# Kernel optimization log

Measured on AMD Instinct MI355X. Metric: run time of the kernel, lower is better.

Reference implementation:

```python
import jax, jax.numpy as jnp
import numpy as np

H = 1024   # hidden size
E = 8      # num experts
B, S = 4, 2048


def setup_inputs() -> dict:
    key = jax.random.key(0)
    k1, k2, k3, k4 = jax.random.split(key, 4)
    x = jax.random.normal(k1, (B, S, H), dtype=jnp.float32)
    wg = jax.random.normal(k2, (H, E), dtype=jnp.float32) * 0.02      # gate weight
    W = jax.random.normal(k3, (E, H, H), dtype=jnp.float32) * 0.02    # expert Linear weights (out, in) per expert
    b = jax.random.normal(k4, (E, H), dtype=jnp.float32) * 0.02       # expert Linear biases
    return {"x": x, "wg": wg, "W": W, "b": b}


def reference(x, wg, W, b):
    Bb, Ss, Hh = x.shape
    Ee = wg.shape[1]
    T = Bb * Ss
    C = T // Ee  # capacity (capacity_factor = 1.0, top-1)

    xt = x.reshape(T, Hh)
    logits = xt @ wg                                   # [T, E]
    probs = jax.nn.softmax(logits, axis=-1)            # [T, E]
    idx = jnp.argmax(probs, axis=-1)                   # [T] top-1 expert
    mask = jax.nn.one_hot(idx, Ee, dtype=xt.dtype)     # [T, E]

    # position of each token within its expert's queue (0-based)
    locations = jnp.cumsum(mask, axis=0) - mask        # [T, E]
    # drop tokens over capacity
    mask = mask * (locations < C).astype(xt.dtype)
    gate = jnp.sum(probs * mask, axis=-1)              # [T] gate prob (0 if dropped)
    loc_s = jnp.sum(locations * mask, axis=-1).astype(jnp.int32)  # [T]
    loc_oh = jax.nn.one_hot(loc_s, C, dtype=xt.dtype)  # [T, C]

    dispatch = mask[:, :, None] * loc_oh[:, None, :]   # [T, E, C]
    combine = gate[:, None, None] * dispatch           # [T, E, C]

    # dispatch tokens -> per-expert buffers [E, C, H]
    exp_in = jnp.einsum('tec,th->ech', dispatch, xt)
    # per-expert Linear: y = x @ W_e^T + b_e
    exp_out = jnp.einsum('ech,efh->ecf', exp_in, W) + b[:, None, :]
    # combine back to tokens, scaled by gate prob
    out = jnp.einsum('tec,ecf->tf', combine, exp_out)  # [T, H]
    return out.reshape(Bb, Ss, Hh)
```

## Files before the change

### kernel.cpp

```cpp
#include <hip/hip_runtime.h>

#define H 1024
#define E 8
#define T 8192
#define CAP 1024

typedef __bf16 bf16x8 __attribute__((ext_vector_type(8)));
typedef float  f32x4  __attribute__((ext_vector_type(4)));
typedef unsigned short u16;

__device__ __forceinline__ u16 f2bf(float f) {
    union { float f; unsigned u; } v; v.f = f;
    unsigned r = v.u + 0x7FFFu + ((v.u >> 16) & 1u);
    return (u16)(r >> 16);
}

typedef __attribute__((address_space(1))) const void* gas_t;
typedef __attribute__((address_space(3))) void* las_t;
__device__ __forceinline__ void gld16(const void* g, void* l) {
    __builtin_amdgcn_global_load_lds((gas_t)g, (las_t)l, 16, 0, 0);
}

__global__ __launch_bounds__(256) void wgt_kernel(
    const float* __restrict__ wg, float* __restrict__ wgT) {
    const int h = blockIdx.x * 256 + threadIdx.x;
    float4 lo = *(const float4*)(wg + h * E);
    float4 hi = *(const float4*)(wg + h * E + 4);
    wgT[0 * H + h] = lo.x; wgT[1 * H + h] = lo.y;
    wgT[2 * H + h] = lo.z; wgT[3 * H + h] = lo.w;
    wgT[4 * H + h] = hi.x; wgT[5 * H + h] = hi.y;
    wgT[6 * H + h] = hi.z; wgT[7 * H + h] = hi.w;
}

#define GATE_BLOCKS 512
#define CVT_BLOCKS  1536

__global__ __launch_bounds__(256) void gatecvt_kernel(
    const float* __restrict__ x, const float* __restrict__ wgT,
    const float* __restrict__ W,
    int* __restrict__ eid, float* __restrict__ gate,
    u16* __restrict__ xbf, u16* __restrict__ Wbf) {
    const int tid = threadIdx.x;

    if (blockIdx.x >= GATE_BLOCKS) {
        int i = (blockIdx.x - GATE_BLOCKS) * 256 + tid;
        const int n4 = E * H * H / 4;
        const int stride = CVT_BLOCKS * 256;
        for (; i < n4; i += stride) {
            float4 v = ((const float4*)W)[i];
            ushort4 o;
            o.x = f2bf(v.x); o.y = f2bf(v.y); o.z = f2bf(v.z); o.w = f2bf(v.w);
            ((ushort4*)Wbf)[i] = o;
        }
        return;
    }

    const int wv = tid >> 6, lane = tid & 63;
    const int tbase = blockIdx.x * 16 + wv * 4;
    const int h00 = lane * 4;

    float a[4][8];
    #pragma unroll
    for (int j = 0; j < 4; ++j)
        #pragma unroll
        for (int e = 0; e < 8; ++e) a[j][e] = 0.f;

    #pragma unroll
    for (int q = 0; q < 4; ++q) {
        const int h0 = q * 256 + h00;
        float4 xv[4];
        #pragma unroll
        for (int j = 0; j < 4; ++j)
            xv[j] = *(const float4*)(x + (size_t)(tbase + j) * H + h0);
        #pragma unroll
        for (int j = 0; j < 4; ++j) {
            ushort4 o;
            o.x = f2bf(xv[j].x); o.y = f2bf(xv[j].y);
            o.z = f2bf(xv[j].z); o.w = f2bf(xv[j].w);
            *(ushort4*)(xbf + (size_t)(tbase + j) * H + h0) = o;
        }
        #pragma unroll
        for (int e = 0; e < 8; ++e) {
            const float4 w4 = *(const float4*)(wgT + e * H + h0);
            #pragma unroll
            for (int j = 0; j < 4; ++j)
                a[j][e] += xv[j].x * w4.x + xv[j].y * w4.y
                         + xv[j].z * w4.z + xv[j].w * w4.w;
        }
    }

    const bool b0 = lane & 1, b1 = lane & 2, b2 = lane & 4;
    const int elane = ((lane & 1) << 2) | (lane & 2) | ((lane >> 2) & 1);

    #pragma unroll
    for (int j = 0; j < 4; ++j) {
        float* A = a[j];
        #pragma unroll
        for (int k = 0; k < 4; ++k) {
            float t = b0 ? A[k] : A[k + 4];
            t = __shfl_xor(t, 1);
            A[k] = (b0 ? A[k + 4] : A[k]) + t;
        }
        #pragma unroll
        for (int k = 0; k < 2; ++k) {
            float t = b1 ? A[k] : A[k + 2];
            t = __shfl_xor(t, 2);
            A[k] = (b1 ? A[k + 2] : A[k]) + t;
        }
        {
            float t = b2 ? A[0] : A[1];
            t = __shfl_xor(t, 4);
            A[0] = (b2 ? A[1] : A[0]) + t;
        }
        float v = A[0];
        v += __shfl_xor(v, 8); v += __shfl_xor(v, 16); v += __shfl_xor(v, 32);
        float m = v; int mi = elane;
        #pragma unroll
        for (int off = 1; off <= 4; off <<= 1) {
            float om = __shfl_xor(m, off);
            int   oi = __shfl_xor(mi, off);
            if (om > m || (om == m && oi < mi)) { m = om; mi = oi; }
        }
        float s = expf(v - m);
        s += __shfl_xor(s, 1); s += __shfl_xor(s, 2); s += __shfl_xor(s, 4);
        if (lane == 0) {
            eid[tbase + j]  = mi;
            gate[tbase + j] = 1.0f / s;
        }
    }
}

#define TPT 32
__global__ __launch_bounds__(256) void scan_kernel(
    const int* __restrict__ eid, float* __restrict__ gate,
    int* __restrict__ perm) {
    __shared__ int cnt[256][E];
    __shared__ int base[256][E];
    __shared__ int part[E][8];
    const int tid = threadIdx.x;

    for (int i = tid; i < E * CAP; i += 256) perm[i] = -1;

    const int t0 = tid * TPT;
    int c[E];
    #pragma unroll
    for (int e = 0; e < E; ++e) c[e] = 0;
    for (int i = 0; i < TPT; ++i) {
        const int ei = eid[t0 + i];
        #pragma unroll
        for (int e = 0; e < E; ++e) c[e] += (ei == e);
    }
    #pragma unroll
    for (int e = 0; e < E; ++e) cnt[tid][e] = c[e];
    __syncthreads();
    if (tid < 64) {
        const int e = tid >> 3, j = tid & 7;
        int s = 0;
        for (int i = j * 32; i < j * 32 + 32; ++i) s += cnt[i][e];
        part[e][j] = s;
    }
    __syncthreads();
    if (tid < E) {
        int run = 0;
        #pragma unroll
        for (int j = 0; j < 8; ++j) { int v = part[tid][j]; part[tid][j] = run; run += v; }
    }
    __syncthreads();
    if (tid < 64) {
        const int e = tid >> 3, j = tid & 7;
        int run = part[e][j];
        for (int i = j * 32; i < j * 32 + 32; ++i) { base[i][e] = run; run += cnt[i][e]; }
    }
    __syncthreads();
    #pragma unroll
    for (int e = 0; e < E; ++e) c[e] = base[tid][e];
    for (int i = 0; i < TPT; ++i) {
        const int t = t0 + i;
        const int ei = eid[t];
        int pos = 0;
        #pragma unroll
        for (int e = 0; e < E; ++e) if (ei == e) pos = c[e]++;
        if (pos < CAP) perm[ei * CAP + pos] = t;
        else gate[t] = 0.f;
    }
}

__global__ __launch_bounds__(512, 4) void moe_gemm_bf(
    const u16* __restrict__ xbf, const u16* __restrict__ Wbf,
    const float* __restrict__ bias, const int* __restrict__ perm,
    const float* __restrict__ gate, float* __restrict__ out) {
    __shared__ __align__(16) u16 As[2][128 * 64];
    __shared__ __align__(16) u16 Bs[2][128 * 64];
    __shared__ int   perm_s[128];
    __shared__ float gate_s[128];

    const int tid = threadIdx.x;
    const int idx = blockIdx.x;

    if (idx >= 512) {
        const int t = (idx - 512) * 128 + (tid >> 2);
        if (gate[t] == 0.f) {
            const int part = tid & 3;
            float4 z = make_float4(0.f, 0.f, 0.f, 0.f);
            float4* o = (float4*)(out + (size_t)t * H + part * 256);
            #pragma unroll
            for (int i = 0; i < 64; ++i) o[i] = z;
        }
        return;
    }

    const int fb = idx >> 6;
    const int mb = (idx >> 3) & 7;
    const int e  = idx & 7;

    if (tid < 128) {
        const int t = perm[e * CAP + mb * 128 + tid];
        perm_s[tid] = t;
        gate_s[tid] = (t >= 0) ? gate[t] : 0.f;
    }
    __syncthreads();

    const int lane = tid & 63;
    const int wv = tid >> 6;
    const int wm = wv >> 2;
    const int wn = wv & 3;
    const int l16 = lane & 15, quad = lane >> 4;

    const int rl  = lane >> 3;
    const int cch = lane & 7;
    const int gch = cch ^ rl;
    const u16* ga[2]; const u16* gb[2];
    #pragma unroll
    for (int q = 0; q < 2; ++q) {
        const int r = wv * 16 + q * 8 + rl;
        const int tA = perm_s[r];
        const int tok = tA >= 0 ? tA : 0;
        ga[q] = xbf + (size_t)tok * H + gch * 8;
        gb[q] = Wbf + (size_t)e * H * H + (size_t)(fb * 128 + r) * H + gch * 8;
    }

    f32x4 acc[4][2] = {};

    for (int kt = 0; kt < H / 128; ++kt) {
        __syncthreads();
        #pragma unroll
        for (int hb = 0; hb < 2; ++hb)
            #pragma unroll
            for (int q = 0; q < 2; ++q) {
                u16* la = &As[hb][(wv * 16 + q * 8) * 64 + lane * 8];
                u16* lb = &Bs[hb][(wv * 16 + q * 8) * 64 + lane * 8];
                gld16(ga[q] + hb * 64, la);
                gld16(gb[q] + hb * 64, lb);
            }
        #pragma unroll
        for (int q = 0; q < 2; ++q) { ga[q] += 128; gb[q] += 128; }
        __syncthreads();
        #pragma unroll
        for (int hb = 0; hb < 2; ++hb)
            #pragma unroll
            for (int s = 0; s < 2; ++s) {
                bf16x8 af[4], bfr[2];
                const int cc = (s * 4 + quad) ^ (l16 & 7);
                #pragma unroll
                for (int i = 0; i < 4; ++i)
                    af[i] = *(const bf16x8*)&As[hb][(wm * 64 + i * 16 + l16) * 64 + cc * 8];
                #pragma unroll
                for (int i = 0; i < 2; ++i)
                    bfr[i] = *(const bf16x8*)&Bs[hb][(wn * 32 + i * 16 + l16) * 64 + cc * 8];
                #pragma unroll
                for (int mi = 0; mi < 4; ++mi)
                    #pragma unroll
                    for (int ni = 0; ni < 2; ++ni)
                        acc[mi][ni] = __builtin_amdgcn_mfma_f32_16x16x32_bf16(
                            af[mi], bfr[ni], acc[mi][ni], 0, 0, 0);
            }
    }

    float bv[2];
    #pragma unroll
    for (int ni = 0; ni < 2; ++ni)
        bv[ni] = bias[e * H + fb * 128 + wn * 32 + ni * 16 + l16];

    #pragma unroll
    for (int mi = 0; mi < 4; ++mi) {
        #pragma unroll
        for (int r = 0; r < 4; ++r) {
            const int rowl = wm * 64 + mi * 16 + quad * 4 + r;
            const int t = perm_s[rowl];
            if (t < 0) continue;
            const float g = gate_s[rowl];
            float* orow = out + (size_t)t * H + fb * 128 + wn * 32;
            #pragma unroll
            for (int ni = 0; ni < 2; ++ni)
                orow[ni * 16 + l16] = g * (acc[mi][ni][r] + bv[ni]);
        }
    }
}

extern "C" void kernel_launch(void* const* d_in, const int* in_sizes, int n_in,
                              void* d_out, int out_size, void* d_ws, size_t ws_size,
                              hipStream_t stream) {
    const float* x    = (const float*)d_in[0];
    const float* wg   = (const float*)d_in[1];
    const float* W    = (const float*)d_in[2];
    const float* bias = (const float*)d_in[3];
    float* out = (float*)d_out;

    int*   eid  = (int*)d_ws;
    float* gate = (float*)((char*)d_ws + (size_t)T * 4);
    int*   perm = (int*)((char*)d_ws + (size_t)T * 8);
    float* wgT  = (float*)((char*)d_ws + (size_t)T * 12);
    u16*   xbf  = (u16*)((char*)d_ws + (size_t)T * 12 + (size_t)E * H * 4);
    u16*   Wbf  = xbf + (size_t)T * H;

    wgt_kernel<<<H / 256, 256, 0, stream>>>(wg, wgT);
    gatecvt_kernel<<<GATE_BLOCKS + CVT_BLOCKS, 256, 0, stream>>>(
        x, wgT, W, eid, gate, xbf, Wbf);
    scan_kernel<<<1, 256, 0, stream>>>(eid, gate, perm);
    moe_gemm_bf<<<512 + 64, 512, 0, stream>>>(xbf, Wbf, bias, perm, gate, out);
}
```

Measured before the change: 152.5 us.

## Convert expert weights to bf16 inside GEMM and drop separate conversion pass

Removes the standalone fp32-to-bf16 conversion of the 32 MB expert weight tensor. The GEMM now loads fp32 weights into registers one k-tile ahead, packs them with v_cvt_pk_bf16_f32 and stores them to LDS, which avoids writing and re-reading a 16 MB bf16 copy. The gate weight transpose is folded into the gate kernel through shared memory, the scan is widened to 1024 threads, and the zero-fill blocks are moved to the front of the grid. Each weight tile is now read as fp32 once per token block (8 m-blocks per expert), which doubles B-side global traffic and adds register pressure and conversion work inside the GEMM loop.

```diff
diff --git a/kernel.cpp b/kernel.cpp
--- a/kernel.cpp
+++ b/kernel.cpp
@@ -15,45 +15,43 @@
     return (u16)(r >> 16);
 }
 
+__device__ __forceinline__ unsigned cvt2bf(float lo, float hi) {
+    unsigned r;
+    asm("v_cvt_pk_bf16_f32 %0, %1, %2" : "=v"(r) : "v"(lo), "v"(hi));
+    return r;
+}
+
 typedef __attribute__((address_space(1))) const void* gas_t;
 typedef __attribute__((address_space(3))) void* las_t;
 __device__ __forceinline__ void gld16(const void* g, void* l) {
     __builtin_amdgcn_global_load_lds((gas_t)g, (las_t)l, 16, 0, 0);
 }
 
-__global__ __launch_bounds__(256) void wgt_kernel(
-    const float* __restrict__ wg, float* __restrict__ wgT) {
-    const int h = blockIdx.x * 256 + threadIdx.x;
-    float4 lo = *(const float4*)(wg + h * E);
-    float4 hi = *(const float4*)(wg + h * E + 4);
-    wgT[0 * H + h] = lo.x; wgT[1 * H + h] = lo.y;
-    wgT[2 * H + h] = lo.z; wgT[3 * H + h] = lo.w;
-    wgT[4 * H + h] = hi.x; wgT[5 * H + h] = hi.y;
-    wgT[6 * H + h] = hi.z; wgT[7 * H + h] = hi.w;
-}
-
-#define GATE_BLOCKS 512
-#define CVT_BLOCKS  1536
-
-__global__ __launch_bounds__(256) void gatecvt_kernel(
-    const float* __restrict__ x, const float* __restrict__ wgT,
-    const float* __restrict__ W,
-    int* __restrict__ eid, float* __restrict__ gate,
-    u16* __restrict__ xbf, u16* __restrict__ Wbf) {
+__global__ __launch_bounds__(256) void gate_kernel(
+    const float* __restrict__ x, const float* __restrict__ wg,
+    int* __restrict__ eid, float* __restrict__ gate, u16* __restrict__ xbf) {
+    __shared__ float wgs[E][H];
     const int tid = threadIdx.x;
 
-    if (blockIdx.x >= GATE_BLOCKS) {
-        int i = (blockIdx.x - GATE_BLOCKS) * 256 + tid;
-        const int n4 = E * H * H / 4;
-        const int stride = CVT_BLOCKS * 256;
-        for (; i < n4; i += stride) {
-            float4 v = ((const float4*)W)[i];
-            ushort4 o;
-            o.x = f2bf(v.x); o.y = f2bf(v.y); o.z = f2bf(v.z); o.w = f2bf(v.w);
-            ((ushort4*)Wbf)[i] = o;
-        }
-        return;
-    }
+    {
+        const int h0 = tid * 4;
+        float4 lo[4], hi[4];
+        #pragma unroll
+        for (int r = 0; r < 4; ++r) {
+            const float4* p = (const float4*)(wg + (size_t)(h0 + r) * E);
+            lo[r] = p[0]; hi[r] = p[1];
+        }
+        #pragma unroll
+        for (int e = 0; e < 4; ++e) {
+            float4 v0 = make_float4(((const float*)&lo[0])[e], ((const float*)&lo[1])[e],
+                                    ((const float*)&lo[2])[e], ((const float*)&lo[3])[e]);
+            *(float4*)&wgs[e][h0] = v0;
+            float4 v1 = make_float4(((const float*)&hi[0])[e], ((const float*)&hi[1])[e],
+                                    ((const float*)&hi[2])[e], ((const float*)&hi[3])[e]);
+            *(float4*)&wgs[e + 4][h0] = v1;
+        }
+    }
+    __syncthreads();
 
     const int wv = tid >> 6, lane = tid & 63;
     const int tbase = blockIdx.x * 16 + wv * 4;
@@ -81,7 +79,7 @@
         }
         #pragma unroll
         for (int e = 0; e < 8; ++e) {
-            const float4 w4 = *(const float4*)(wgT + e * H + h0);
+            const float4 w4 = *(const float4*)&wgs[e][h0];
             #pragma unroll
             for (int j = 0; j < 4; ++j)
                 a[j][e] += xv[j].x * w4.x + xv[j].y * w4.y
@@ -130,63 +128,68 @@
     }
 }
 
-#define TPT 32
-__global__ __launch_bounds__(256) void scan_kernel(
+#define SCAN_T 1024
+#define STPT 8
+__global__ __launch_bounds__(1024) void scan_kernel(
     const int* __restrict__ eid, float* __restrict__ gate,
     int* __restrict__ perm) {
-    __shared__ int cnt[256][E];
-    __shared__ int base[256][E];
-    __shared__ int part[E][8];
+    __shared__ int cnt[SCAN_T][E];
+    __shared__ int part[E][32];
     const int tid = threadIdx.x;
 
-    for (int i = tid; i < E * CAP; i += 256) perm[i] = -1;
-
-    const int t0 = tid * TPT;
+    for (int i = tid; i < E * CAP; i += SCAN_T) perm[i] = -1;
+
+    const int t0 = tid * STPT;
+    int ei[STPT];
+    #pragma unroll
+    for (int i = 0; i < STPT; ++i) ei[i] = eid[t0 + i];
+
     int c[E];
     #pragma unroll
     for (int e = 0; e < E; ++e) c[e] = 0;
-    for (int i = 0; i < TPT; ++i) {
-        const int ei = eid[t0 + i];
-        #pragma unroll
-        for (int e = 0; e < E; ++e) c[e] += (ei == e);
-    }
+    #pragma unroll
+    for (int i = 0; i < STPT; ++i)
+        #pragma unroll
+        for (int e = 0; e < E; ++e) c[e] += (ei[i] == e);
     #pragma unroll
     for (int e = 0; e < E; ++e) cnt[tid][e] = c[e];
     __syncthreads();
-    if (tid < 64) {
-        const int e = tid >> 3, j = tid & 7;
+
+    if (tid < 256) {
+        const int e = tid >> 5, g = tid & 31;
         int s = 0;
-        for (int i = j * 32; i < j * 32 + 32; ++i) s += cnt[i][e];
-        part[e][j] = s;
+        for (int i = g * 32; i < g * 32 + 32; ++i) s += cnt[i][e];
+        part[e][g] = s;
     }
     __syncthreads();
     if (tid < E) {
         int run = 0;
         #pragma unroll
-        for (int j = 0; j < 8; ++j) { int v = part[tid][j]; part[tid][j] = run; run += v; }
-    }
-    __syncthreads();
-    if (tid < 64) {
-        const int e = tid >> 3, j = tid & 7;
-        int run = part[e][j];
-        for (int i = j * 32; i < j * 32 + 32; ++i) { base[i][e] = run; run += cnt[i][e]; }
-    }
-    __syncthreads();
-    #pragma unroll
-    for (int e = 0; e < E; ++e) c[e] = base[tid][e];
-    for (int i = 0; i < TPT; ++i) {
-        const int t = t0 + i;
-        const int ei = eid[t];
+        for (int g = 0; g < 32; ++g) { int v = part[tid][g]; part[tid][g] = run; run += v; }
+    }
+    __syncthreads();
+    if (tid < 256) {
+        const int e = tid >> 5, g = tid & 31;
+        int run = part[e][g];
+        for (int i = g * 32; i < g * 32 + 32; ++i) { int v = cnt[i][e]; cnt[i][e] = run; run += v; }
+    }
+    __syncthreads();
+
+    #pragma unroll
+    for (int e = 0; e < E; ++e) c[e] = cnt[tid][e];
+    #pragma unroll
+    for (int i = 0; i < STPT; ++i) {
+        const int t = t0 + i, e0 = ei[i];
         int pos = 0;
         #pragma unroll
-        for (int e = 0; e < E; ++e) if (ei == e) pos = c[e]++;
-        if (pos < CAP) perm[ei * CAP + pos] = t;
+        for (int k = 0; k < E; ++k) if (e0 == k) pos = c[k]++;
+        if (pos < CAP) perm[e0 * CAP + pos] = t;
         else gate[t] = 0.f;
     }
 }
 
 __global__ __launch_bounds__(512, 4) void moe_gemm_bf(
-    const u16* __restrict__ xbf, const u16* __restrict__ Wbf,
+    const u16* __restrict__ xbf, const float* __restrict__ W,
     const float* __restrict__ bias, const int* __restrict__ perm,
     const float* __restrict__ gate, float* __restrict__ out) {
     __shared__ __align__(16) u16 As[2][128 * 64];
@@ -195,10 +198,10 @@
     __shared__ float gate_s[128];
 
     const int tid = threadIdx.x;
-    const int idx = blockIdx.x;
-
-    if (idx >= 512) {
-        const int t = (idx - 512) * 128 + (tid >> 2);
+    const int bid = blockIdx.x;
+
+    if (bid < 64) {
+        const int t = bid * 128 + (tid >> 2);
         if (gate[t] == 0.f) {
             const int part = tid & 3;
             float4 z = make_float4(0.f, 0.f, 0.f, 0.f);
@@ -209,6 +212,7 @@
         return;
     }
 
+    const int idx = bid - 64;
     const int fb = idx >> 6;
     const int mb = (idx >> 3) & 7;
     const int e  = idx & 7;
@@ -229,17 +233,31 @@
     const int rl  = lane >> 3;
     const int cch = lane & 7;
     const int gch = cch ^ rl;
-    const u16* ga[2]; const u16* gb[2];
+    const u16*   ga[2];
+    const float* gb[2];
     #pragma unroll
     for (int q = 0; q < 2; ++q) {
         const int r = wv * 16 + q * 8 + rl;
         const int tA = perm_s[r];
         const int tok = tA >= 0 ? tA : 0;
         ga[q] = xbf + (size_t)tok * H + gch * 8;
-        gb[q] = Wbf + (size_t)e * H * H + (size_t)(fb * 128 + r) * H + gch * 8;
+        gb[q] = W + (size_t)e * H * H + (size_t)(fb * 128 + r) * H + gch * 8;
     }
 
     f32x4 acc[4][2] = {};
+
+    uint4 pw[4];
+    #pragma unroll
+    for (int hb = 0; hb < 2; ++hb)
+        #pragma unroll
+        for (int q = 0; q < 2; ++q) {
+            const float4* p = (const float4*)(gb[q] + hb * 64);
+            const float4 v0 = p[0], v1 = p[1];
+            uint4 v;
+            v.x = cvt2bf(v0.x, v0.y); v.y = cvt2bf(v0.z, v0.w);
+            v.z = cvt2bf(v1.x, v1.y); v.w = cvt2bf(v1.z, v1.w);
+            pw[hb * 2 + q] = v;
+        }
 
     for (int kt = 0; kt < H / 128; ++kt) {
         __syncthreads();
@@ -248,13 +266,31 @@
             #pragma unroll
             for (int q = 0; q < 2; ++q) {
                 u16* la = &As[hb][(wv * 16 + q * 8) * 64 + lane * 8];
-                u16* lb = &Bs[hb][(wv * 16 + q * 8) * 64 + lane * 8];
                 gld16(ga[q] + hb * 64, la);
-                gld16(gb[q] + hb * 64, lb);
             }
+        #pragma unroll
+        for (int hb = 0; hb < 2; ++hb)
+            #pragma unroll
+            for (int q = 0; q < 2; ++q)
+                *(uint4*)&Bs[hb][(wv * 16 + q * 8 + rl) * 64 + cch * 8] = pw[hb * 2 + q];
         #pragma unroll
         for (int q = 0; q < 2; ++q) { ga[q] += 128; gb[q] += 128; }
         __syncthreads();
+
+        if (kt < H / 128 - 1) {
+            #pragma unroll
+            for (int hb = 0; hb < 2; ++hb)
+                #pragma unroll
+                for (int q = 0; q < 2; ++q) {
+                    const float4* p = (const float4*)(gb[q] + hb * 64);
+                    const float4 v0 = p[0], v1 = p[1];
+                    uint4 v;
+                    v.x = cvt2bf(v0.x, v0.y); v.y = cvt2bf(v0.z, v0.w);
+                    v.z = cvt2bf(v1.x, v1.y); v.w = cvt2bf(v1.z, v1.w);
+                    pw[hb * 2 + q] = v;
+                }
+        }
+
         #pragma unroll
         for (int hb = 0; hb < 2; ++hb)
             #pragma unroll
@@ -309,13 +345,9 @@
     int*   eid  = (int*)d_ws;
     float* gate = (float*)((char*)d_ws + (size_t)T * 4);
     int*   perm = (int*)((char*)d_ws + (size_t)T * 8);
-    float* wgT  = (float*)((char*)d_ws + (size_t)T * 12);
-    u16*   xbf  = (u16*)((char*)d_ws + (size_t)T * 12 + (size_t)E * H * 4);
-    u16*   Wbf  = xbf + (size_t)T * H;
-
-    wgt_kernel<<<H / 256, 256, 0, stream>>>(wg, wgT);
-    gatecvt_kernel<<<GATE_BLOCKS + CVT_BLOCKS, 256, 0, stream>>>(
-        x, wgT, W, eid, gate, xbf, Wbf);
-    scan_kernel<<<1, 256, 0, stream>>>(eid, gate, perm);
-    moe_gemm_bf<<<512 + 64, 512, 0, stream>>>(xbf, Wbf, bias, perm, gate, out);
-}
+    u16*   xbf  = (u16*)((char*)d_ws + (size_t)T * 12);
+
+    gate_kernel<<<T / 16, 256, 0, stream>>>(x, wg, eid, gate, xbf);
+    scan_kernel<<<1, SCAN_T, 0, stream>>>(eid, gate, perm);
+    moe_gemm_bf<<<64 + 512, 512, 0, stream>>>(xbf, W, bias, perm, gate, out);
+}
```

New measurement: 159.4 us. 4.5% more time.
